# Optimization experiments

Hardware: AMD Instinct MI355X
Metric: run time of the kernel (lower is better)

## Reference

```python
import jax, jax.numpy as jnp
import numpy as np

TEMP = 0.05
BG_KNN = 50
POSK = 3
BAL_W = 0.15
P = 32768   # num proxies in memory bank
D = 256     # feature dim
C = 8       # num cameras (proxy p has camera p % C, pseudo-label p // C)
N = 65536   # dataset size
B = 256     # batch


def setup_inputs() -> dict:
    key = jax.random.key(0)
    k1, k2, k3, k4 = jax.random.split(key, 4)
    mem = jax.random.normal(k1, (P, D), jnp.float32)
    mem = mem / jnp.linalg.norm(mem, axis=1, keepdims=True)  # L2-normalized bank
    features = jax.random.normal(k2, (B, D), jnp.float32)
    all_proxy_label = jax.random.randint(k3, (N,), 0, P, jnp.int32)
    all_pseudo_label = all_proxy_label // C          # consistent with label_proxies layout
    targets = jax.random.randint(k4, (B,), 0, N, jnp.int32)
    cams = all_proxy_label[targets] % C              # each sample's camera owns its target proxy
    Pc = P // C
    cam_proxies = (jnp.arange(C)[:, None] + C * jnp.arange(Pc)[None, :]).astype(jnp.int32)   # [C, Pc]
    label_proxies = (jnp.arange(P // C)[:, None] * C + jnp.arange(C)[None, :]).astype(jnp.int32)  # [num_ids, C]
    return dict(features=features, targets=targets, cams=cams, epoch=0,
                global_memory=mem, all_pseudo_label=all_pseudo_label,
                all_proxy_label=all_proxy_label, cam_proxies=cam_proxies,
                label_proxies=label_proxies)


def _cam_mean_sum(per_sample, cams, num_cams):
    # original: for each camera, mean loss over that camera's samples, then sum over cameras
    s = jax.ops.segment_sum(per_sample, cams, num_segments=num_cams)
    n = jax.ops.segment_sum(jnp.ones_like(per_sample), cams, num_segments=num_cams)
    return jnp.where(n > 0, s / jnp.maximum(n, 1.0), 0.0).sum()


def _forward(features, global_memory, targets, cams, all_pseudo_label,
             all_proxy_label, cam_proxies, label_proxies):
    pseudo_y = all_pseudo_label[targets]      # [B]
    prx = all_proxy_label[targets]            # [B]
    num_cams = cam_proxies.shape[0]
    Bsz = features.shape[0]
    rows = jnp.arange(Bsz)

    # ExemplarMemory: score = features @ memory^T; backward treats memory as constant
    score = features @ jax.lax.stop_gradient(global_memory).T   # [B, P]
    inputs = score / TEMP

    # --- intra-camera loss: log-softmax over this sample's camera proxies ---
    cam_prx = cam_proxies[cams]                                   # [B, Pc]
    sel = jnp.take_along_axis(inputs, cam_prx, axis=1)            # [B, Pc]
    mask = (cam_prx == prx[:, None]).astype(inputs.dtype)
    intra = -(jax.nn.log_softmax(sel, axis=1) * mask).sum(axis=1)

    # --- cross-camera proxy-associate loss: positives + bg_knn hardest negatives ---
    pos = label_proxies[pseudo_y]                                 # [B, K]
    K = pos.shape[1]
    temp = jax.lax.stop_gradient(inputs).at[rows[:, None], pos].set(10000.0)
    _, top_idx = jax.lax.top_k(temp, BG_KNN + K)                  # descending: positives first
    sel2 = jnp.take_along_axis(inputs, top_idx, axis=1)           # [B, bg_knn+K]
    tgt2 = jnp.concatenate([jnp.full((K,), 1.0 / K, inputs.dtype),
                            jnp.zeros((BG_KNN,), inputs.dtype)])
    cross = -(jax.nn.log_softmax(sel2, axis=1) * tgt2).sum(axis=1)

    # --- online camera-wise NN-enhance loss ---
    mem = jax.lax.stop_gradient(global_memory)
    sims = BAL_W * jax.lax.stop_gradient(score) + (1.0 - BAL_W) * (mem[prx] @ mem.T)  # [B, P]
    sims_by_cam = sims[:, cam_proxies]                            # [B, C, Pc]
    arg = jnp.argmax(sims_by_cam, axis=2)                         # [B, C] best proxy per camera
    tops = cam_proxies[jnp.arange(num_cams)[None, :], arg]        # [B, C]
    top_vals = jnp.take_along_axis(sims, tops, axis=1)            # [B, C]
    _, sel_c = jax.lax.top_k(top_vals, POSK)                      # posK strongest camera-tops
    chosen = jnp.take_along_axis(tops, sel_c, axis=1)             # [B, posK]
    sims = sims.at[rows[:, None], chosen].set(10000.0)
    _, top3 = jax.lax.top_k(sims, BG_KNN + POSK)                  # positives first (descending)
    sel3 = jnp.take_along_axis(inputs, top3, axis=1)
    tgt3 = jnp.concatenate([jnp.full((POSK,), 1.0 / POSK, inputs.dtype),
                            jnp.zeros((BG_KNN,), inputs.dtype)])
    online = -(jax.nn.log_softmax(sel3, axis=1) * tgt3).sum(axis=1)

    return (_cam_mean_sum(intra, cams, num_cams)
            + _cam_mean_sum(cross, cams, num_cams)
            + _cam_mean_sum(online, cams, num_cams))


def reference(features, targets, cams, epoch, global_memory, all_pseudo_label,
              all_proxy_label, cam_proxies, label_proxies):
    return _forward(features, global_memory, targets, cams,
                    all_pseudo_label, all_proxy_label, cam_proxies, label_proxies)
```

## Files before the change

kernel.cpp:

```cpp
#include <hip/hip_runtime.h>

#define P_CNT 32768
#define D_DIM 256
#define B_SZ  256
#define NTHR  1024
#define NW    16
#define INVT  20.0f
#define NEG_BIG -3.0e38f

typedef _Float16 half8  __attribute__((ext_vector_type(8)));
typedef _Float16 half4v __attribute__((ext_vector_type(4)));
typedef float    floatx4 __attribute__((ext_vector_type(4)));

__device__ __forceinline__ float blockMax(float v, int tid, float* redW) {
#pragma unroll
  for (int off = 1; off < 64; off <<= 1) v = fmaxf(v, __shfl_xor(v, off));
  if ((tid & 63) == 0) redW[tid >> 6] = v;
  __syncthreads();
  float r = redW[0];
#pragma unroll
  for (int w = 1; w < NW; ++w) r = fmaxf(r, redW[w]);
  __syncthreads();
  return r;
}

__device__ __forceinline__ float blockSum(float v, int tid, float* redW) {
#pragma unroll
  for (int off = 1; off < 64; off <<= 1) v += __shfl_xor(v, off);
  if ((tid & 63) == 0) redW[tid >> 6] = v;
  __syncthreads();
  float r = 0.f;
#pragma unroll
  for (int w = 0; w < NW; ++w) r += redW[w];
  __syncthreads();
  return r;
}

template <typename GetV>
__device__ __forceinline__ float histSelectK(GetV getv, int k, int tid,
                                             int* hist , int* wt ,
                                             int* ibc , float* bufV ,
                                             int* cntS, float* bcast) {
  const int lane = tid & 63, wid = tid >> 6;
  int shift = 19, prevShift = 32;
  unsigned prefix = 0;
  int krem = k;
  for (;;) {
    {
      int4* h4 = (int4*)hist;
      h4[tid] = make_int4(0, 0, 0, 0);
      h4[tid + 1024] = make_int4(0, 0, 0, 0);
    }
    __syncthreads();
#pragma unroll
    for (int j = 0; j < 32; ++j) {
      float v = getv(j);
      unsigned bu = __float_as_uint(v);
      unsigned key = bu ^ ((unsigned)(((int)bu) >> 31) | 0x80000000u);
      bool ok = (prevShift >= 32) || ((key >> prevShift) == prefix);
      if (ok) atomicAdd(&hist[(key >> shift) & 8191], 1);
    }
    __syncthreads();
    int bcnt[8];
    int L = 0;
#pragma unroll
    for (int j = 0; j < 8; ++j) { bcnt[j] = hist[8 * tid + j]; L += bcnt[j]; }
    int S = L;
#pragma unroll
    for (int off = 1; off < 64; off <<= 1) {
      int y = __shfl_down(S, off);
      S += (lane + off < 64) ? y : 0;
    }
    if (lane == 0) wt[wid] = S;
    __syncthreads();
    int aboveW = 0;
    for (int w = wid + 1; w < NW; ++w) aboveW += wt[w];
    const int R = S + aboveW;
    const int aboveR = R - L;
    if (aboveR < krem && krem <= R) {
      int above = aboveR;
      int bsel = -1, csel = 0;
#pragma unroll
      for (int j = 7; j >= 0; --j) {
        if (bsel < 0) {
          if (above + bcnt[j] >= krem) { bsel = 8 * tid + j; csel = bcnt[j]; }
          else above += bcnt[j];
        }
      }
      ibc[0] = bsel; ibc[1] = krem - above; ibc[2] = csel;
    }
    __syncthreads();
    const int bstar = ibc[0];
    krem = ibc[1];
    const int cntT = ibc[2];
    __syncthreads();
    const int gap = prevShift - shift;
    prefix = (prefix << gap) | ((unsigned)bstar & ((1u << gap) - 1u));
    prevShift = shift;
    if (cntT <= 64 || shift == 0) break;
    shift = (shift >= 13) ? (shift - 13) : 0;
  }
  if (tid == 0) cntS[0] = 0;
  __syncthreads();
#pragma unroll
  for (int j = 0; j < 32; ++j) {
    float v = getv(j);
    unsigned bu = __float_as_uint(v);
    unsigned key = bu ^ ((unsigned)(((int)bu) >> 31) | 0x80000000u);
    if ((key >> prevShift) == prefix) {
      int p = atomicAdd(cntS, 1);
      if (p < 64) bufV[p] = v;
    }
  }
  __syncthreads();
  if (tid < 64) {
    int n = min(cntS[0], 64);
    float vl = (tid < n) ? bufV[tid] : NEG_BIG;
    float vkv = NEG_BIG;
    for (int it = 0; it < krem; ++it) {
      float wv = vl;
#pragma unroll
      for (int off = 1; off < 64; off <<= 1) wv = fmaxf(wv, __shfl_xor(wv, off));
      if (it == krem - 1) vkv = wv;
      unsigned long long m = __ballot(vl == wv);
      int fl = (int)__ffsll(m) - 1;
      if (tid == fl) vl = NEG_BIG;
    }
    if (tid == 0) bcast[0] = vkv;
  }
  __syncthreads();
  float r = bcast[0];
  __syncthreads();
  return r;
}

__global__ void prep_kernel(const float* __restrict__ features,
                            const int* __restrict__ targets,
                            const int* __restrict__ all_prx,
                            const float* __restrict__ mem,
                            float* __restrict__ A2,
                            int* __restrict__ prxArr) {
  const int b = blockIdx.x;
  const int k = threadIdx.x;
  const int t = targets[b];
  const int pr = all_prx[t];
  if (k == 0) prxArr[b] = pr;
  A2[b * D_DIM + k] = features[b * D_DIM + k];
  A2[(B_SZ + b) * D_DIM + k] = mem[(size_t)pr * D_DIM + k];
}

__global__ __launch_bounds__(256) void gemm_mfma(const float* __restrict__ A,
                                                 const float* __restrict__ Bm,
                                                 float* __restrict__ Co) {
  __shared__ _Float16 Ah[128][32], Al[128][32], Bh[128][32], Bl[128][32];
  const int tid = threadIdx.x;
  const int lane = tid & 63;
  const int wid = tid >> 6;
  const int wr = wid >> 1, wc = wid & 1;
  const int orig = (blockIdx.x & 7) * 128 + (blockIdx.x >> 3);
  const int rowBase = (orig & 3) << 7;
  const int colBase = (orig >> 2) << 7;

  const int trow = tid >> 3;
  const int tseg = tid & 7;

  floatx4 acc[4][4];
#pragma unroll
  for (int i = 0; i < 4; ++i)
#pragma unroll
    for (int j = 0; j < 4; ++j) {
      acc[i][j][0] = 0.f; acc[i][j][1] = 0.f; acc[i][j][2] = 0.f; acc[i][j][3] = 0.f;
    }

  const int fr = lane & 15;
  const int kg = (lane >> 4) << 3;

  for (int step = 0; step < 8; ++step) {
    const int k0 = step << 5;
    float4 sa[4], sb[4];
#pragma unroll
    for (int p = 0; p < 4; ++p) {
      const int r = trow + (p << 5);
      sa[p] = *(const float4*)(A  + (size_t)(rowBase + r) * D_DIM + k0 + tseg * 4);
      sb[p] = *(const float4*)(Bm + (size_t)(colBase + r) * D_DIM + k0 + tseg * 4);
    }
    __syncthreads();
#pragma unroll
    for (int p = 0; p < 4; ++p) {
      const int r = trow + (p << 5);
      float4 v = sa[p];
      half4v h, l;
      h[0] = (_Float16)v.x; l[0] = (_Float16)(v.x - (float)h[0]);
      h[1] = (_Float16)v.y; l[1] = (_Float16)(v.y - (float)h[1]);
      h[2] = (_Float16)v.z; l[2] = (_Float16)(v.z - (float)h[2]);
      h[3] = (_Float16)v.w; l[3] = (_Float16)(v.w - (float)h[3]);
      *(half4v*)&Ah[r][tseg * 4] = h;
      *(half4v*)&Al[r][tseg * 4] = l;
      v = sb[p];
      h[0] = (_Float16)v.x; l[0] = (_Float16)(v.x - (float)h[0]);
      h[1] = (_Float16)v.y; l[1] = (_Float16)(v.y - (float)h[1]);
      h[2] = (_Float16)v.z; l[2] = (_Float16)(v.z - (float)h[2]);
      h[3] = (_Float16)v.w; l[3] = (_Float16)(v.w - (float)h[3]);
      *(half4v*)&Bh[r][tseg * 4] = h;
      *(half4v*)&Bl[r][tseg * 4] = l;
    }
    __syncthreads();
    half8 ah[4], al[4], bh[4], bl[4];
#pragma unroll
    for (int f = 0; f < 4; ++f) {
      ah[f] = *(const half8*)&Ah[wr * 64 + f * 16 + fr][kg];
      al[f] = *(const half8*)&Al[wr * 64 + f * 16 + fr][kg];
      bh[f] = *(const half8*)&Bh[wc * 64 + f * 16 + fr][kg];
      bl[f] = *(const half8*)&Bl[wc * 64 + f * 16 + fr][kg];
    }
#pragma unroll
    for (int fm = 0; fm < 4; ++fm)
#pragma unroll
      for (int fn = 0; fn < 4; ++fn) {
        acc[fm][fn] = __builtin_amdgcn_mfma_f32_16x16x32_f16(ah[fm], bh[fn], acc[fm][fn], 0, 0, 0);
        acc[fm][fn] = __builtin_amdgcn_mfma_f32_16x16x32_f16(ah[fm], bl[fn], acc[fm][fn], 0, 0, 0);
        acc[fm][fn] = __builtin_amdgcn_mfma_f32_16x16x32_f16(al[fm], bh[fn], acc[fm][fn], 0, 0, 0);
      }
  }
  const int rsub = (lane >> 4) << 2;
#pragma unroll
  for (int fm = 0; fm < 4; ++fm)
#pragma unroll
    for (int fn = 0; fn < 4; ++fn) {
      const int r0 = rowBase + wr * 64 + fm * 16 + rsub;
      const int c0 = colBase + wc * 64 + fn * 16 + fr;
#pragma unroll
      for (int r = 0; r < 4; ++r)
        Co[(size_t)(r0 + r) * P_CNT + c0] = acc[fm][fn][r];
    }
}

__global__ __launch_bounds__(NTHR) void persample(const float* __restrict__ OUT,
                                                  const int* __restrict__ cams,
                                                  const int* __restrict__ prxArr,
                                                  float* __restrict__ intraArr,
                                                  float* __restrict__ crossArr,
                                                  float* __restrict__ onlArr) {
  __shared__ int   hist[8192];
  __shared__ int   wt[NW];
  __shared__ int   ibc[4];
  __shared__ float bufV[64];
  __shared__ int   bufI[32];
  __shared__ int   cntS[4];
  __shared__ float redW[NW];
  __shared__ float sv[64];
  __shared__ int   si[64];
  __shared__ float cvW[NW * 8];
  __shared__ int   ciW[NW * 8];
  __shared__ float mw[NW], sw[NW];
  __shared__ float bcast[2];

  const int b = blockIdx.x;
  const int tid = threadIdx.x;
  const int lane = tid & 63, wid = tid >> 6;
  const float* Srow = OUT + (size_t)b * P_CNT;
  const float* Mrow = OUT + (size_t)(B_SZ + b) * P_CNT;
  const int pr = prxArr[b];
  const int cam = cams[b];
  const int base4 = tid << 2;

  float s[32];
#pragma unroll
  for (int q = 0; q < 8; ++q) {
    float4 f = ((const float4*)Srow)[tid + (q << 10)];
    s[4 * q + 0] = f.x; s[4 * q + 1] = f.y; s[4 * q + 2] = f.z; s[4 * q + 3] = f.w;
  }
  float pmax = NEG_BIG;
#pragma unroll
  for (int j = 0; j < 32; ++j) pmax = fmaxf(pmax, s[j]);
  const float M = blockMax(pmax, tid, redW);

  {
    const bool mine = ((tid & 1) == (cam >> 2));
    const int cc = cam & 3;
    float im = NEG_BIG, is = 0.f;
    if (mine) {
#pragma unroll
      for (int q = 0; q < 8; ++q) {
        float v = (cc == 0) ? s[4 * q] : (cc == 1) ? s[4 * q + 1]
                : (cc == 2) ? s[4 * q + 2] : s[4 * q + 3];
        if (v <= im) is += expf((v - im) * INVT);
        else { is = is * expf((im - v) * INVT) + 1.f; im = v; }
      }
    }
#pragma unroll
    for (int off = 1; off < 64; off <<= 1) {
      float m2 = __shfl_xor(im, off);
      float s2 = __shfl_xor(is, off);
      float Mx = fmaxf(im, m2);
      is = is * expf((im - Mx) * INVT) + s2 * expf((m2 - Mx) * INVT);
      im = Mx;
    }
    if (lane == 0) { mw[wid] = im; sw[wid] = is; }
  }
  __syncthreads();
  if (tid == 0) {
    float m0 = mw[0], s0 = sw[0];
    for (int w = 1; w < NW; ++w) {
      float Mx = fmaxf(m0, mw[w]);
      s0 = s0 * expf((m0 - Mx) * INVT) + sw[w] * expf((mw[w] - Mx) * INVT);
      m0 = Mx;
    }
    intraArr[b] = -((Srow[pr] - m0) * INVT - logf(s0));
  }

  const int posBase = pr & ~7;
  if (tid < 8) sv[tid] = Srow[posBase + tid];
  __syncthreads();
  auto crossVal = [&](int j) -> float {
    int p = base4 + ((j >> 2) << 12) + (j & 3);
    return ((unsigned)(p - posBase) < 8u) ? NEG_BIG : s[j];
  };
  const float vk = histSelectK(crossVal, 50, tid, hist, wt, ibc, bufV, cntS, bcast);
  {
    float se = 0.f, cg = 0.f;
#pragma unroll
    for (int j = 0; j < 32; ++j) {
      float v = crossVal(j);
      if (v > vk) { se += expf((v - M) * INVT); cg += 1.f; }
    }
    se = blockSum(se, tid, redW);
    cg = blockSum(cg, tid, redW);
    if (tid == 0) {
      float stot = se + (50.f - cg) * expf((vk - M) * INVT);
      for (int p = 0; p < 8; ++p) stot += expf((sv[p] - M) * INVT);
      float lse = logf(stot);
      float acc = 0.f;
      for (int p = 0; p < 8; ++p) acc += (sv[p] - M) * INVT - lse;
      crossArr[b] = -acc * 0.125f;
    }
  }

#pragma unroll
  for (int q = 0; q < 8; ++q) {
    float4 m2 = ((const float4*)Mrow)[tid + (q << 10)];
    s[4 * q + 0] = 0.15f * s[4 * q + 0] + 0.85f * m2.x;
    s[4 * q + 1] = 0.15f * s[4 * q + 1] + 0.85f * m2.y;
    s[4 * q + 2] = 0.15f * s[4 * q + 2] + 0.85f * m2.z;
    s[4 * q + 3] = 0.15f * s[4 * q + 3] + 0.85f * m2.w;
  }

  {
    float cm[4] = {NEG_BIG, NEG_BIG, NEG_BIG, NEG_BIG};
    int cix[4] = {0x7fffffff, 0x7fffffff, 0x7fffffff, 0x7fffffff};
#pragma unroll
    for (int q = 0; q < 8; ++q) {
#pragma unroll
      for (int c = 0; c < 4; ++c) {
        float v = s[4 * q + c];
        int p = base4 + (q << 12) + c;
        if (v > cm[c]) { cm[c] = v; cix[c] = p; }
      }
    }
    const bool odd = (tid & 1);
    float v8[8]; int i8[8];
#pragma unroll
    for (int c = 0; c < 4; ++c) {
      float ov = __shfl_xor(cm[c], 1); int oi = __shfl_xor(cix[c], 1);
      v8[c]     = odd ? ov : cm[c];   i8[c]     = odd ? oi : cix[c];
      v8[c + 4] = odd ? cm[c] : ov;   i8[c + 4] = odd ? cix[c] : oi;
    }
#pragma unroll
    for (int off = 2; off <= 32; off <<= 1) {
#pragma unroll
      for (int c = 0; c < 8; ++c) {
        float vv = __shfl_xor(v8[c], off);
        int   ii = __shfl_xor(i8[c], off);
        if (vv > v8[c] || (vv == v8[c] && ii < i8[c])) { v8[c] = vv; i8[c] = ii; }
      }
    }
    if (lane < 8) {
#pragma unroll
      for (int c = 0; c < 8; ++c)
        if (lane == c) { cvW[wid * 8 + c] = v8[c]; ciW[wid * 8 + c] = i8[c]; }
    }
    __syncthreads();
    if (tid < 8) {
      float v = cvW[tid]; int ix = ciW[tid];
      for (int w = 1; w < NW; ++w) {
        float v2 = cvW[w * 8 + tid]; int i2 = ciW[w * 8 + tid];
        if (v2 > v || (v2 == v && i2 < ix)) { v = v2; ix = i2; }
      }
      cvW[tid] = v; ciW[tid] = ix;
    }
    __syncthreads();
    if (tid == 0) {
      unsigned used = 0;
      for (int k = 0; k < 3; ++k) {
        float best = NEG_BIG; int bc = 0;
        for (int c = 0; c < 8; ++c)
          if (!((used >> c) & 1u) && cvW[c] > best) { best = cvW[c]; bc = c; }
        used |= 1u << bc;
        si[k] = ciW[bc];
      }
    }
    __syncthreads();
  }
  const int c0 = si[0], c1 = si[1], c2 = si[2];
  __syncthreads();

  auto simsVal = [&](int j) -> float {
    int p = base4 + ((j >> 2) << 12) + (j & 3);
    return (p == c0 || p == c1 || p == c2) ? NEG_BIG : s[j];
  };
  const float vk2 = histSelectK(simsVal, 50, tid, hist, wt, ibc, bufV, cntS, bcast);
  if (tid == 0) { cntS[1] = 0; cntS[2] = 0; }
  __syncthreads();
#pragma unroll
  for (int j = 0; j < 32; ++j) {
    float v = simsVal(j);
    int p = base4 + ((j >> 2) << 12) + (j & 3);
    if (v > vk2) {
      int t = atomicAdd(&cntS[1], 1);
      if (t < 50) si[3 + t] = p;
    } else if (v == vk2) {
      int t = atomicAdd(&cntS[2], 1);
      if (t < 32) bufI[t] = p;
    }
  }
  __syncthreads();
  {
    const int cg = cntS[1];
    const int fill = 50 - cg;
    if (tid < 64) {
      int ne = min(cntS[2], 32);
      int il = (tid < ne) ? bufI[tid] : 0x7fffffff;
      for (int it = 0; it < fill; ++it) {
        int wi = il;
#pragma unroll
        for (int off = 1; off < 64; off <<= 1) wi = min(wi, __shfl_xor(wi, off));
        if (tid == 0) si[3 + cg + it] = wi;
        if (il == wi) il = 0x7fffffff;
      }
    }
  }
  __syncthreads();
  if (tid < 53) sv[tid] = Srow[si[tid]];
  __syncthreads();
  if (tid < 64) {
    float v = (tid < 53) ? sv[tid] : NEG_BIG;
    float mm = v;
#pragma unroll
    for (int off = 1; off < 64; off <<= 1) mm = fmaxf(mm, __shfl_xor(mm, off));
    float e = (tid < 53) ? expf((v - mm) * INVT) : 0.f;
    float ss = e;
#pragma unroll
    for (int off = 1; off < 64; off <<= 1) ss += __shfl_xor(ss, off);
    float lse = logf(ss);
    float c = (tid < 3) ? ((v - mm) * INVT - lse) : 0.f;
#pragma unroll
    for (int off = 1; off < 64; off <<= 1) c += __shfl_xor(c, off);
    if (tid == 0) onlArr[b] = -c * (1.0f / 3.0f);
  }
}

__global__ void finalize(const int* __restrict__ cams,
                         const float* __restrict__ ia,
                         const float* __restrict__ ca,
                         const float* __restrict__ oa,
                         float* __restrict__ out) {
  if (blockIdx.x == 0 && threadIdx.x == 0) {
    float s[8] = {}; float n[8] = {};
    for (int b = 0; b < B_SZ; ++b) {
      int c = cams[b];
      s[c] += ia[b] + ca[b] + oa[b];
      n[c] += 1.f;
    }
    float tot = 0.f;
    for (int c = 0; c < 8; ++c)
      if (n[c] > 0.f) tot += s[c] / n[c];
    out[0] = tot;
  }
}

extern "C" void kernel_launch(void* const* d_in, const int* in_sizes, int n_in,
                              void* d_out, int out_size, void* d_ws, size_t ws_size,
                              hipStream_t stream) {
  const float* features = (const float*)d_in[0];
  const int*   targets  = (const int*)d_in[1];
  const int*   cams     = (const int*)d_in[2];
  const float* mem      = (const float*)d_in[4];
  const int*   all_prx  = (const int*)d_in[6];

  float* ws = (float*)d_ws;
  float* A2  = ws;
  float* OUT = ws + 512 * D_DIM;
  float* tail = OUT + (size_t)512 * P_CNT;
  int*   prxArr  = (int*)tail;
  float* intraArr = (float*)(prxArr + B_SZ);
  float* crossArr = intraArr + B_SZ;
  float* onlArr   = crossArr + B_SZ;

  prep_kernel<<<B_SZ, D_DIM, 0, stream>>>(features, targets, all_prx, mem, A2, prxArr);
  gemm_mfma<<<1024, 256, 0, stream>>>(A2, mem, OUT);
  persample<<<B_SZ, NTHR, 0, stream>>>(OUT, cams, prxArr, intraArr, crossArr, onlArr);
  finalize<<<1, 64, 0, stream>>>(cams, intraArr, crossArr, onlArr, (float*)d_out);
}
```

Baseline: 143.7 us.

## Fuse top-k threshold selection with candidate gathering to cut block syncs

Splits the histogram radix select so it returns only the target bin prefix. The final pass then gathers above-bin elements directly and the in-bin candidates into shared buffers. The k-th value is resolved by a one-wave rank count over at most 64 candidates instead of a serial extract-max loop. This drops one full 32-element rescan per selection and several block-wide barriers and reductions, and the online loss tail now runs within a single wave. A reader note: the in-wave write to si followed by reading Srow[si[tid]] relies on wave-level ordering of shared memory without a barrier, and candidates beyond 64 are silently dropped.

```diff
diff --git a/kernel.cpp b/kernel.cpp
--- a/kernel.cpp
+++ b/kernel.cpp
@@ -36,27 +36,29 @@
   return r;
 }
 
+__device__ __forceinline__ unsigned fkey(float v) {
+  unsigned bu = __float_as_uint(v);
+  return bu ^ ((unsigned)(((int)bu) >> 31) | 0x80000000u);
+}
+
 template <typename GetV>
-__device__ __forceinline__ float histSelectK(GetV getv, int k, int tid,
-                                             int* hist , int* wt ,
-                                             int* ibc , float* bufV ,
-                                             int* cntS, float* bcast) {
+__device__ __forceinline__ void histFindBin(GetV getv, int k, int tid,
+                                            int* hist , int* wt ,
+                                            int* ibc ,
+                                            unsigned& prefixOut, int& prevShiftOut,
+                                            int& kremOut) {
   const int lane = tid & 63, wid = tid >> 6;
   int shift = 19, prevShift = 32;
   unsigned prefix = 0;
   int krem = k;
   for (;;) {
-    {
-      int4* h4 = (int4*)hist;
-      h4[tid] = make_int4(0, 0, 0, 0);
-      h4[tid + 1024] = make_int4(0, 0, 0, 0);
-    }
+    int4* h4 = (int4*)hist;
+    h4[tid] = make_int4(0, 0, 0, 0);
+    h4[tid + 1024] = make_int4(0, 0, 0, 0);
     __syncthreads();
 #pragma unroll
     for (int j = 0; j < 32; ++j) {
-      float v = getv(j);
-      unsigned bu = __float_as_uint(v);
-      unsigned key = bu ^ ((unsigned)(((int)bu) >> 31) | 0x80000000u);
+      unsigned key = fkey(getv(j));
       bool ok = (prevShift >= 32) || ((key >> prevShift) == prefix);
       if (ok) atomicAdd(&hist[(key >> shift) & 8191], 1);
     }
@@ -93,45 +95,14 @@
     const int bstar = ibc[0];
     krem = ibc[1];
     const int cntT = ibc[2];
-    __syncthreads();
     const int gap = prevShift - shift;
     prefix = (prefix << gap) | ((unsigned)bstar & ((1u << gap) - 1u));
     prevShift = shift;
     if (cntT <= 64 || shift == 0) break;
     shift = (shift >= 13) ? (shift - 13) : 0;
-  }
-  if (tid == 0) cntS[0] = 0;
-  __syncthreads();
-#pragma unroll
-  for (int j = 0; j < 32; ++j) {
-    float v = getv(j);
-    unsigned bu = __float_as_uint(v);
-    unsigned key = bu ^ ((unsigned)(((int)bu) >> 31) | 0x80000000u);
-    if ((key >> prevShift) == prefix) {
-      int p = atomicAdd(cntS, 1);
-      if (p < 64) bufV[p] = v;
-    }
-  }
-  __syncthreads();
-  if (tid < 64) {
-    int n = min(cntS[0], 64);
-    float vl = (tid < n) ? bufV[tid] : NEG_BIG;
-    float vkv = NEG_BIG;
-    for (int it = 0; it < krem; ++it) {
-      float wv = vl;
-#pragma unroll
-      for (int off = 1; off < 64; off <<= 1) wv = fmaxf(wv, __shfl_xor(wv, off));
-      if (it == krem - 1) vkv = wv;
-      unsigned long long m = __ballot(vl == wv);
-      int fl = (int)__ffsll(m) - 1;
-      if (tid == fl) vl = NEG_BIG;
-    }
-    if (tid == 0) bcast[0] = vkv;
-  }
-  __syncthreads();
-  float r = bcast[0];
-  __syncthreads();
-  return r;
+    __syncthreads();
+  }
+  prefixOut = prefix; prevShiftOut = prevShift; kremOut = krem;
 }
 
 __global__ void prep_kernel(const float* __restrict__ features,
@@ -245,7 +216,7 @@
   __shared__ int   wt[NW];
   __shared__ int   ibc[4];
   __shared__ float bufV[64];
-  __shared__ int   bufI[32];
+  __shared__ int   bufI[64];
   __shared__ int   cntS[4];
   __shared__ float redW[NW];
   __shared__ float sv[64];
@@ -253,7 +224,6 @@
   __shared__ float cvW[NW * 8];
   __shared__ int   ciW[NW * 8];
   __shared__ float mw[NW], sw[NW];
-  __shared__ float bcast[2];
 
   const int b = blockIdx.x;
   const int tid = threadIdx.x;
@@ -298,6 +268,8 @@
     }
     if (lane == 0) { mw[wid] = im; sw[wid] = is; }
   }
+  const int posBase = pr & ~7;
+  if (tid < 8) sv[tid] = Srow[posBase + tid];
   __syncthreads();
   if (tid == 0) {
     float m0 = mw[0], s0 = sw[0];
@@ -309,30 +281,51 @@
     intraArr[b] = -((Srow[pr] - m0) * INVT - logf(s0));
   }
 
-  const int posBase = pr & ~7;
-  if (tid < 8) sv[tid] = Srow[posBase + tid];
-  __syncthreads();
   auto crossVal = [&](int j) -> float {
     int p = base4 + ((j >> 2) << 12) + (j & 3);
     return ((unsigned)(p - posBase) < 8u) ? NEG_BIG : s[j];
   };
-  const float vk = histSelectK(crossVal, 50, tid, hist, wt, ibc, bufV, cntS, bcast);
   {
-    float se = 0.f, cg = 0.f;
+    unsigned prefix; int prevShift, krem;
+    histFindBin(crossVal, 50, tid, hist, wt, ibc, prefix, prevShift, krem);
+    if (tid == 0) cntS[0] = 0;
+    __syncthreads();
+    float seAbove = 0.f;
 #pragma unroll
     for (int j = 0; j < 32; ++j) {
       float v = crossVal(j);
-      if (v > vk) { se += expf((v - M) * INVT); cg += 1.f; }
-    }
-    se = blockSum(se, tid, redW);
-    cg = blockSum(cg, tid, redW);
-    if (tid == 0) {
-      float stot = se + (50.f - cg) * expf((vk - M) * INVT);
-      for (int p = 0; p < 8; ++p) stot += expf((sv[p] - M) * INVT);
-      float lse = logf(stot);
-      float acc = 0.f;
-      for (int p = 0; p < 8; ++p) acc += (sv[p] - M) * INVT - lse;
-      crossArr[b] = -acc * 0.125f;
+      unsigned keyTop = fkey(v) >> prevShift;
+      if (keyTop > prefix) seAbove += expf((v - M) * INVT);
+      else if (keyTop == prefix) {
+        int p = atomicAdd(&cntS[0], 1);
+        if (p < 64) bufV[p] = v;
+      }
+    }
+    seAbove = blockSum(seAbove, tid, redW);
+    if (tid < 64) {
+      const int n = min(cntS[0], 64);
+      const bool valid = (tid < n);
+      float vl = valid ? bufV[tid] : NEG_BIG;
+      int r = 0, eq = 0;
+      for (int m2 = 0; m2 < 64; ++m2) {
+        float vm = (m2 < n) ? bufV[m2] : NEG_BIG;
+        r += (vm > vl); eq += (vm == vl);
+      }
+      unsigned long long mb = __ballot(valid && r < krem && krem <= r + eq);
+      int selLane = (mb == 0) ? 0 : (int)__ffsll(mb) - 1;
+      float vk = __shfl(vl, selLane);
+      int rAbove = __shfl(r, selLane);
+      float e = (valid && vl > vk) ? expf((vl - M) * INVT) : 0.f;
+#pragma unroll
+      for (int off = 1; off < 64; off <<= 1) e += __shfl_xor(e, off);
+      if (tid == 0) {
+        float stot = seAbove + e + (float)(krem - rAbove) * expf((vk - M) * INVT);
+        float acc = 0.f;
+        for (int p = 0; p < 8; ++p) stot += expf((sv[p] - M) * INVT);
+        float lse = logf(stot);
+        for (int p = 0; p < 8; ++p) acc += (sv[p] - M) * INVT - lse;
+        crossArr[b] = -acc * 0.125f;
+      }
     }
   }
 
@@ -408,54 +401,62 @@
     int p = base4 + ((j >> 2) << 12) + (j & 3);
     return (p == c0 || p == c1 || p == c2) ? NEG_BIG : s[j];
   };
-  const float vk2 = histSelectK(simsVal, 50, tid, hist, wt, ibc, bufV, cntS, bcast);
-  if (tid == 0) { cntS[1] = 0; cntS[2] = 0; }
-  __syncthreads();
-#pragma unroll
-  for (int j = 0; j < 32; ++j) {
-    float v = simsVal(j);
-    int p = base4 + ((j >> 2) << 12) + (j & 3);
-    if (v > vk2) {
-      int t = atomicAdd(&cntS[1], 1);
-      if (t < 50) si[3 + t] = p;
-    } else if (v == vk2) {
-      int t = atomicAdd(&cntS[2], 1);
-      if (t < 32) bufI[t] = p;
-    }
-  }
-  __syncthreads();
   {
-    const int cg = cntS[1];
-    const int fill = 50 - cg;
+    unsigned prefix; int prevShift, krem;
+    histFindBin(simsVal, 50, tid, hist, wt, ibc, prefix, prevShift, krem);
+    if (tid == 0) { cntS[0] = 0; cntS[1] = 3; }
+    __syncthreads();
+#pragma unroll
+    for (int j = 0; j < 32; ++j) {
+      float v = simsVal(j);
+      int p = base4 + ((j >> 2) << 12) + (j & 3);
+      unsigned keyTop = fkey(v) >> prevShift;
+      if (keyTop > prefix) {
+        int t = atomicAdd(&cntS[1], 1);
+        si[t] = p;
+      } else if (keyTop == prefix) {
+        int t = atomicAdd(&cntS[0], 1);
+        if (t < 64) { bufV[t] = v; bufI[t] = p; }
+      }
+    }
+    __syncthreads();
     if (tid < 64) {
-      int ne = min(cntS[2], 32);
-      int il = (tid < ne) ? bufI[tid] : 0x7fffffff;
-      for (int it = 0; it < fill; ++it) {
-        int wi = il;
-#pragma unroll
-        for (int off = 1; off < 64; off <<= 1) wi = min(wi, __shfl_xor(wi, off));
-        if (tid == 0) si[3 + cg + it] = wi;
-        if (il == wi) il = 0x7fffffff;
-      }
-    }
-  }
-  __syncthreads();
-  if (tid < 53) sv[tid] = Srow[si[tid]];
-  __syncthreads();
-  if (tid < 64) {
-    float v = (tid < 53) ? sv[tid] : NEG_BIG;
-    float mm = v;
-#pragma unroll
-    for (int off = 1; off < 64; off <<= 1) mm = fmaxf(mm, __shfl_xor(mm, off));
-    float e = (tid < 53) ? expf((v - mm) * INVT) : 0.f;
-    float ss = e;
-#pragma unroll
-    for (int off = 1; off < 64; off <<= 1) ss += __shfl_xor(ss, off);
-    float lse = logf(ss);
-    float c = (tid < 3) ? ((v - mm) * INVT - lse) : 0.f;
-#pragma unroll
-    for (int off = 1; off < 64; off <<= 1) c += __shfl_xor(c, off);
-    if (tid == 0) onlArr[b] = -c * (1.0f / 3.0f);
+      const int n = min(cntS[0], 64);
+      const bool valid = (tid < n);
+      float vl = valid ? bufV[tid] : NEG_BIG;
+      int il = valid ? bufI[tid] : 0x7fffffff;
+      int r = 0, eq = 0, ti = 0;
+      for (int m2 = 0; m2 < 64; ++m2) {
+        float vm = (m2 < n) ? bufV[m2] : NEG_BIG;
+        int im = (m2 < n) ? bufI[m2] : 0x7fffffff;
+        r += (vm > vl); eq += (vm == vl);
+        ti += (vm == vl && im < il);
+      }
+      unsigned long long mb = __ballot(valid && r < krem && krem <= r + eq);
+      int selLane = (mb == 0) ? 0 : (int)__ffsll(mb) - 1;
+      float vk = __shfl(vl, selLane);
+      int rAbove = __shfl(r, selLane);
+      int tcnt = krem - rAbove;
+      bool take = valid && ((vl > vk) || (vl == vk && ti < tcnt));
+      if (take) {
+        int t = atomicAdd(&cntS[1], 1);
+        si[t] = il;
+      }
+      float v = NEG_BIG;
+      if (tid < 53) v = Srow[si[tid]];
+      float mm = v;
+#pragma unroll
+      for (int off = 1; off < 64; off <<= 1) mm = fmaxf(mm, __shfl_xor(mm, off));
+      float e = (tid < 53) ? expf((v - mm) * INVT) : 0.f;
+      float ss = e;
+#pragma unroll
+      for (int off = 1; off < 64; off <<= 1) ss += __shfl_xor(ss, off);
+      float lse = logf(ss);
+      float c = (tid < 3) ? ((v - mm) * INVT - lse) : 0.f;
+#pragma unroll
+      for (int off = 1; off < 64; off <<= 1) c += __shfl_xor(c, off);
+      if (tid == 0) onlArr[b] = -c * (1.0f / 3.0f);
+    }
   }
 }
 
```

New measurement: 162.6 us. 1.13x slower.

## Split per-sample selection into sliced candidate collection plus merge kernel

Applied to the files above, without the earlier changes.

The single 1024-thread per-sample kernel becomes two stages. The first runs 8 slice blocks per sample and computes partial max and intra-camera logsumexp plus per-camera argmax. It also collects top-K candidates with an adaptive 256-bin value histogram that starts from a guessed range below the slice max. The second kernel merges the slice candidates with a rank-count sort to finish the cross and online losses. This spreads work over more, smaller blocks and replaces the multi-pass radix select, but it relies on value-range heuristics and a fixed candidate cap (128), which could drop correct top-K entries on other data.

```diff
diff --git a/kernel.cpp b/kernel.cpp
--- a/kernel.cpp
+++ b/kernel.cpp
@@ -3,135 +3,105 @@
 #define P_CNT 32768
 #define D_DIM 256
 #define B_SZ  256
-#define NTHR  1024
-#define NW    16
 #define INVT  20.0f
 #define NEG_BIG -3.0e38f
+#define SLICE_N 4096
+#define NSLICE 8
+#define CAP 128
 
 typedef _Float16 half8  __attribute__((ext_vector_type(8)));
 typedef _Float16 half4v __attribute__((ext_vector_type(4)));
 typedef float    floatx4 __attribute__((ext_vector_type(4)));
 
-__device__ __forceinline__ float blockMax(float v, int tid, float* redW) {
+__device__ __forceinline__ float blockMax4(float v, int tid, float* red4) {
 #pragma unroll
   for (int off = 1; off < 64; off <<= 1) v = fmaxf(v, __shfl_xor(v, off));
-  if ((tid & 63) == 0) redW[tid >> 6] = v;
-  __syncthreads();
-  float r = redW[0];
-#pragma unroll
-  for (int w = 1; w < NW; ++w) r = fmaxf(r, redW[w]);
+  if ((tid & 63) == 0) red4[tid >> 6] = v;
+  __syncthreads();
+  float r = fmaxf(fmaxf(red4[0], red4[1]), fmaxf(red4[2], red4[3]));
   __syncthreads();
   return r;
 }
 
-__device__ __forceinline__ float blockSum(float v, int tid, float* redW) {
+__device__ __forceinline__ float blockSum4(float v, int tid, float* red4) {
 #pragma unroll
   for (int off = 1; off < 64; off <<= 1) v += __shfl_xor(v, off);
-  if ((tid & 63) == 0) redW[tid >> 6] = v;
-  __syncthreads();
-  float r = 0.f;
-#pragma unroll
-  for (int w = 0; w < NW; ++w) r += redW[w];
+  if ((tid & 63) == 0) red4[tid >> 6] = v;
+  __syncthreads();
+  float r = red4[0] + red4[1] + red4[2] + red4[3];
   __syncthreads();
   return r;
 }
 
-template <typename GetV>
-__device__ __forceinline__ float histSelectK(GetV getv, int k, int tid,
-                                             int* hist , int* wt ,
-                                             int* ibc , float* bufV ,
-                                             int* cntS, float* bcast) {
-  const int lane = tid & 63, wid = tid >> 6;
-  int shift = 19, prevShift = 32;
-  unsigned prefix = 0;
-  int krem = k;
-  for (;;) {
-    {
-      int4* h4 = (int4*)hist;
-      h4[tid] = make_int4(0, 0, 0, 0);
-      h4[tid + 1024] = make_int4(0, 0, 0, 0);
-    }
-    __syncthreads();
-#pragma unroll
-    for (int j = 0; j < 32; ++j) {
+template <typename GetV, typename GetI>
+__device__ void selectCollect(GetV getv, GetI geti, int K, float hi, float range0,
+                              int tid, int lane,
+                              int* hist, int* ibc, int* lcnt,
+                              float* oVal, int* oIdx, int* oCnt) {
+  float range = range0;
+  for (int guard = 0; guard < 10; ++guard) {
+    const float lo = hi - range;
+    const float scale = 256.0f / range;
+    hist[tid] = 0;
+    if (tid == 0) ibc[0] = -1;
+    __syncthreads();
+#pragma unroll
+    for (int j = 0; j < 16; ++j) {
       float v = getv(j);
-      unsigned bu = __float_as_uint(v);
-      unsigned key = bu ^ ((unsigned)(((int)bu) >> 31) | 0x80000000u);
-      bool ok = (prevShift >= 32) || ((key >> prevShift) == prefix);
-      if (ok) atomicAdd(&hist[(key >> shift) & 8191], 1);
-    }
-    __syncthreads();
-    int bcnt[8];
-    int L = 0;
-#pragma unroll
-    for (int j = 0; j < 8; ++j) { bcnt[j] = hist[8 * tid + j]; L += bcnt[j]; }
-    int S = L;
-#pragma unroll
-    for (int off = 1; off < 64; off <<= 1) {
-      int y = __shfl_down(S, off);
-      S += (lane + off < 64) ? y : 0;
-    }
-    if (lane == 0) wt[wid] = S;
-    __syncthreads();
-    int aboveW = 0;
-    for (int w = wid + 1; w < NW; ++w) aboveW += wt[w];
-    const int R = S + aboveW;
-    const int aboveR = R - L;
-    if (aboveR < krem && krem <= R) {
-      int above = aboveR;
-      int bsel = -1, csel = 0;
-#pragma unroll
-      for (int j = 7; j >= 0; --j) {
-        if (bsel < 0) {
-          if (above + bcnt[j] >= krem) { bsel = 8 * tid + j; csel = bcnt[j]; }
-          else above += bcnt[j];
+      float t = (v - lo) * scale;
+      int bin = (int)fminf(fmaxf(t, 0.0f), 255.0f);
+      if (bin >= 1) atomicAdd(&hist[bin], 1);
+    }
+    __syncthreads();
+    if (tid < 64) {
+      int4 h = ((const int4*)hist)[tid];
+      if (tid == 0) h.x = 0;
+      int L = h.x + h.y + h.z + h.w;
+      int S = L;
+#pragma unroll
+      for (int off = 1; off < 64; off <<= 1) {
+        int y = __shfl_down(S, off);
+        S += (lane + off < 64) ? y : 0;
+      }
+      int total = __shfl(S, 0);
+      if (total >= K) {
+        int above = S - L;
+        if (above < K && S >= K) {
+          int a = above, bsel;
+          if (a + h.w >= K) bsel = 4 * tid + 3;
+          else { a += h.w;
+            if (a + h.z >= K) bsel = 4 * tid + 2;
+            else { a += h.z;
+              if (a + h.y >= K) bsel = 4 * tid + 1;
+              else bsel = 4 * tid;
+            } }
+          ibc[0] = bsel;
         }
       }
-      ibc[0] = bsel; ibc[1] = krem - above; ibc[2] = csel;
-    }
-    __syncthreads();
-    const int bstar = ibc[0];
-    krem = ibc[1];
-    const int cntT = ibc[2];
-    __syncthreads();
-    const int gap = prevShift - shift;
-    prefix = (prefix << gap) | ((unsigned)bstar & ((1u << gap) - 1u));
-    prevShift = shift;
-    if (cntT <= 64 || shift == 0) break;
-    shift = (shift >= 13) ? (shift - 13) : 0;
-  }
-  if (tid == 0) cntS[0] = 0;
-  __syncthreads();
-#pragma unroll
-  for (int j = 0; j < 32; ++j) {
-    float v = getv(j);
-    unsigned bu = __float_as_uint(v);
-    unsigned key = bu ^ ((unsigned)(((int)bu) >> 31) | 0x80000000u);
-    if ((key >> prevShift) == prefix) {
-      int p = atomicAdd(cntS, 1);
-      if (p < 64) bufV[p] = v;
-    }
-  }
-  __syncthreads();
-  if (tid < 64) {
-    int n = min(cntS[0], 64);
-    float vl = (tid < n) ? bufV[tid] : NEG_BIG;
-    float vkv = NEG_BIG;
-    for (int it = 0; it < krem; ++it) {
-      float wv = vl;
-#pragma unroll
-      for (int off = 1; off < 64; off <<= 1) wv = fmaxf(wv, __shfl_xor(wv, off));
-      if (it == krem - 1) vkv = wv;
-      unsigned long long m = __ballot(vl == wv);
-      int fl = (int)__ffsll(m) - 1;
-      if (tid == fl) vl = NEG_BIG;
-    }
-    if (tid == 0) bcast[0] = vkv;
-  }
-  __syncthreads();
-  float r = bcast[0];
-  __syncthreads();
-  return r;
+    }
+    __syncthreads();
+    if (ibc[0] >= 0) {
+      const int Bstar = ibc[0];
+      if (tid == 0) *lcnt = 0;
+      __syncthreads();
+#pragma unroll
+      for (int j = 0; j < 16; ++j) {
+        float v = getv(j);
+        float t = (v - lo) * scale;
+        int bin = (int)fminf(fmaxf(t, 0.0f), 255.0f);
+        if (bin >= Bstar) {
+          int tt = atomicAdd(lcnt, 1);
+          if (tt < CAP) { oVal[tt] = v; oIdx[tt] = geti(j); }
+        }
+      }
+      __syncthreads();
+      if (tid == 0) *oCnt = min(*lcnt, CAP);
+      return;
+    }
+    range *= 4.0f;
+    __syncthreads();
+  }
+  if (tid == 0) *oCnt = 0;
 }
 
 __global__ void prep_kernel(const float* __restrict__ features,
@@ -235,45 +205,40 @@
     }
 }
 
-__global__ __launch_bounds__(NTHR) void persample(const float* __restrict__ OUT,
-                                                  const int* __restrict__ cams,
-                                                  const int* __restrict__ prxArr,
-                                                  float* __restrict__ intraArr,
-                                                  float* __restrict__ crossArr,
-                                                  float* __restrict__ onlArr) {
-  __shared__ int   hist[8192];
-  __shared__ int   wt[NW];
-  __shared__ int   ibc[4];
-  __shared__ float bufV[64];
-  __shared__ int   bufI[32];
-  __shared__ int   cntS[4];
-  __shared__ float redW[NW];
-  __shared__ float sv[64];
-  __shared__ int   si[64];
-  __shared__ float cvW[NW * 8];
-  __shared__ int   ciW[NW * 8];
-  __shared__ float mw[NW], sw[NW];
-  __shared__ float bcast[2];
-
-  const int b = blockIdx.x;
-  const int tid = threadIdx.x;
-  const int lane = tid & 63, wid = tid >> 6;
-  const float* Srow = OUT + (size_t)b * P_CNT;
-  const float* Mrow = OUT + (size_t)(B_SZ + b) * P_CNT;
-  const int pr = prxArr[b];
-  const int cam = cams[b];
-  const int base4 = tid << 2;
-
-  float s[32];
-#pragma unroll
-  for (int q = 0; q < 8; ++q) {
-    float4 f = ((const float4*)Srow)[tid + (q << 10)];
-    s[4 * q + 0] = f.x; s[4 * q + 1] = f.y; s[4 * q + 2] = f.z; s[4 * q + 3] = f.w;
-  }
-  float pmax = NEG_BIG;
-#pragma unroll
-  for (int j = 0; j < 32; ++j) pmax = fmaxf(pmax, s[j]);
-  const float M = blockMax(pmax, tid, redW);
+__global__ __launch_bounds__(256) void persample1(
+    const float* __restrict__ OUT, const int* __restrict__ cams,
+    const int* __restrict__ prxArr,
+    float* __restrict__ pmaxA, float* __restrict__ imA, float* __restrict__ isA,
+    float* __restrict__ camV, int* __restrict__ camI,
+    int* __restrict__ cxCnt, float* __restrict__ cxVal, int* __restrict__ cxIdx,
+    int* __restrict__ smCnt, float* __restrict__ smVal, int* __restrict__ smIdx) {
+  __shared__ __align__(16) int hist[256];
+  __shared__ int ibc[2];
+  __shared__ int lcnt;
+  __shared__ float red4[4];
+  __shared__ float mwS[4], swS[4];
+  __shared__ float cvW[32]; __shared__ int ciW[32];
+
+  const int blk = blockIdx.x;
+  const int b = blk >> 3, s = blk & 7;
+  const int tid = threadIdx.x, lane = tid & 63, wid = tid >> 6;
+  const int sl = b * NSLICE + s;
+  const float* Srow = OUT + (size_t)b * P_CNT + s * SLICE_N;
+  const float* Mrow = OUT + (size_t)(B_SZ + b) * P_CNT + s * SLICE_N;
+  const int pr = prxArr[b], cam = cams[b];
+  const int gbase = s * SLICE_N + 4 * tid;
+
+  float sc[16];
+#pragma unroll
+  for (int q = 0; q < 4; ++q) {
+    float4 f = ((const float4*)Srow)[tid + 256 * q];
+    sc[4 * q + 0] = f.x; sc[4 * q + 1] = f.y; sc[4 * q + 2] = f.z; sc[4 * q + 3] = f.w;
+  }
+  float mx = sc[0];
+#pragma unroll
+  for (int j = 1; j < 16; ++j) mx = fmaxf(mx, sc[j]);
+  const float Mslice = blockMax4(mx, tid, red4);
+  if (tid == 0) pmaxA[sl] = Mslice;
 
   {
     const bool mine = ((tid & 1) == (cam >> 2));
@@ -281,9 +246,9 @@
     float im = NEG_BIG, is = 0.f;
     if (mine) {
 #pragma unroll
-      for (int q = 0; q < 8; ++q) {
-        float v = (cc == 0) ? s[4 * q] : (cc == 1) ? s[4 * q + 1]
-                : (cc == 2) ? s[4 * q + 2] : s[4 * q + 3];
+      for (int q = 0; q < 4; ++q) {
+        float v = (cc == 0) ? sc[4 * q] : (cc == 1) ? sc[4 * q + 1]
+                : (cc == 2) ? sc[4 * q + 2] : sc[4 * q + 3];
         if (v <= im) is += expf((v - im) * INVT);
         else { is = is * expf((im - v) * INVT) + 1.f; im = v; }
       }
@@ -296,67 +261,51 @@
       is = is * expf((im - Mx) * INVT) + s2 * expf((m2 - Mx) * INVT);
       im = Mx;
     }
-    if (lane == 0) { mw[wid] = im; sw[wid] = is; }
-  }
-  __syncthreads();
-  if (tid == 0) {
-    float m0 = mw[0], s0 = sw[0];
-    for (int w = 1; w < NW; ++w) {
-      float Mx = fmaxf(m0, mw[w]);
-      s0 = s0 * expf((m0 - Mx) * INVT) + sw[w] * expf((mw[w] - Mx) * INVT);
-      m0 = Mx;
-    }
-    intraArr[b] = -((Srow[pr] - m0) * INVT - logf(s0));
+    if (lane == 0) { mwS[wid] = im; swS[wid] = is; }
+    __syncthreads();
+    if (tid == 0) {
+      float m0 = mwS[0], s0 = swS[0];
+      for (int w = 1; w < 4; ++w) {
+        float Mx = fmaxf(m0, mwS[w]);
+        s0 = s0 * expf((m0 - Mx) * INVT) + swS[w] * expf((mwS[w] - Mx) * INVT);
+        m0 = Mx;
+      }
+      imA[sl] = m0; isA[sl] = s0;
+    }
+    __syncthreads();
   }
 
   const int posBase = pr & ~7;
-  if (tid < 8) sv[tid] = Srow[posBase + tid];
-  __syncthreads();
-  auto crossVal = [&](int j) -> float {
-    int p = base4 + ((j >> 2) << 12) + (j & 3);
-    return ((unsigned)(p - posBase) < 8u) ? NEG_BIG : s[j];
+  auto cval = [&](int j) -> float {
+    int p = gbase + ((j >> 2) << 10) + (j & 3);
+    return ((unsigned)(p - posBase) < 8u) ? NEG_BIG : sc[j];
   };
-  const float vk = histSelectK(crossVal, 50, tid, hist, wt, ibc, bufV, cntS, bcast);
+  auto gidx = [&](int j) -> int { return gbase + ((j >> 2) << 10) + (j & 3); };
+  selectCollect(cval, gidx, 53, Mslice, 2.0f, tid, lane, hist, ibc, &lcnt,
+                cxVal + (size_t)sl * CAP, cxIdx + (size_t)sl * CAP, cxCnt + sl);
+
+  float sm[16];
+#pragma unroll
+  for (int q = 0; q < 4; ++q) {
+    float4 g = ((const float4*)Mrow)[tid + 256 * q];
+    sm[4 * q + 0] = 0.15f * sc[4 * q + 0] + 0.85f * g.x;
+    sm[4 * q + 1] = 0.15f * sc[4 * q + 1] + 0.85f * g.y;
+    sm[4 * q + 2] = 0.15f * sc[4 * q + 2] + 0.85f * g.z;
+    sm[4 * q + 3] = 0.15f * sc[4 * q + 3] + 0.85f * g.w;
+  }
+
   {
-    float se = 0.f, cg = 0.f;
-#pragma unroll
-    for (int j = 0; j < 32; ++j) {
-      float v = crossVal(j);
-      if (v > vk) { se += expf((v - M) * INVT); cg += 1.f; }
-    }
-    se = blockSum(se, tid, redW);
-    cg = blockSum(cg, tid, redW);
-    if (tid == 0) {
-      float stot = se + (50.f - cg) * expf((vk - M) * INVT);
-      for (int p = 0; p < 8; ++p) stot += expf((sv[p] - M) * INVT);
-      float lse = logf(stot);
-      float acc = 0.f;
-      for (int p = 0; p < 8; ++p) acc += (sv[p] - M) * INVT - lse;
-      crossArr[b] = -acc * 0.125f;
-    }
-  }
-
-#pragma unroll
-  for (int q = 0; q < 8; ++q) {
-    float4 m2 = ((const float4*)Mrow)[tid + (q << 10)];
-    s[4 * q + 0] = 0.15f * s[4 * q + 0] + 0.85f * m2.x;
-    s[4 * q + 1] = 0.15f * s[4 * q + 1] + 0.85f * m2.y;
-    s[4 * q + 2] = 0.15f * s[4 * q + 2] + 0.85f * m2.z;
-    s[4 * q + 3] = 0.15f * s[4 * q + 3] + 0.85f * m2.w;
-  }
-
-  {
-    float cm[4] = {NEG_BIG, NEG_BIG, NEG_BIG, NEG_BIG};
-    int cix[4] = {0x7fffffff, 0x7fffffff, 0x7fffffff, 0x7fffffff};
-#pragma unroll
-    for (int q = 0; q < 8; ++q) {
+    float cm[4]; int cix[4];
+#pragma unroll
+    for (int c = 0; c < 4; ++c) { cm[c] = NEG_BIG; cix[c] = 0x7fffffff; }
+#pragma unroll
+    for (int q = 0; q < 4; ++q)
 #pragma unroll
       for (int c = 0; c < 4; ++c) {
-        float v = s[4 * q + c];
-        int p = base4 + (q << 12) + c;
+        float v = sm[4 * q + c];
+        int p = gbase + (q << 10) + c;
         if (v > cm[c]) { cm[c] = v; cix[c] = p; }
       }
-    }
     const bool odd = (tid & 1);
     float v8[8]; int i8[8];
 #pragma unroll
@@ -366,14 +315,12 @@
       v8[c + 4] = odd ? cm[c] : ov;   i8[c + 4] = odd ? cix[c] : oi;
     }
 #pragma unroll
-    for (int off = 2; off <= 32; off <<= 1) {
+    for (int off = 2; off <= 32; off <<= 1)
 #pragma unroll
       for (int c = 0; c < 8; ++c) {
-        float vv = __shfl_xor(v8[c], off);
-        int   ii = __shfl_xor(i8[c], off);
+        float vv = __shfl_xor(v8[c], off); int ii = __shfl_xor(i8[c], off);
         if (vv > v8[c] || (vv == v8[c] && ii < i8[c])) { v8[c] = vv; i8[c] = ii; }
       }
-    }
     if (lane < 8) {
 #pragma unroll
       for (int c = 0; c < 8; ++c)
@@ -382,80 +329,200 @@
     __syncthreads();
     if (tid < 8) {
       float v = cvW[tid]; int ix = ciW[tid];
-      for (int w = 1; w < NW; ++w) {
+      for (int w = 1; w < 4; ++w) {
         float v2 = cvW[w * 8 + tid]; int i2 = ciW[w * 8 + tid];
         if (v2 > v || (v2 == v && i2 < ix)) { v = v2; ix = i2; }
       }
-      cvW[tid] = v; ciW[tid] = ix;
-    }
-    __syncthreads();
+      camV[(size_t)sl * 8 + tid] = v; camI[(size_t)sl * 8 + tid] = ix;
+    }
+    __syncthreads();
+  }
+
+  float mx2 = sm[0];
+#pragma unroll
+  for (int j = 1; j < 16; ++j) mx2 = fmaxf(mx2, sm[j]);
+  const float Ms = blockMax4(mx2, tid, red4);
+  auto sval = [&](int j) -> float { return sm[j]; };
+  selectCollect(sval, gidx, 56, Ms, 0.35f, tid, lane, hist, ibc, &lcnt,
+                smVal + (size_t)sl * CAP, smIdx + (size_t)sl * CAP, smCnt + sl);
+}
+
+__global__ __launch_bounds__(256) void persample2(
+    const float* __restrict__ OUT, const int* __restrict__ prxArr,
+    const float* __restrict__ pmaxA, const float* __restrict__ imA,
+    const float* __restrict__ isA,
+    const float* __restrict__ camV, const int* __restrict__ camI,
+    const int* __restrict__ cxCnt, const float* __restrict__ cxVal,
+    const int* __restrict__ cxIdx,
+    const int* __restrict__ smCnt, const float* __restrict__ smVal,
+    const int* __restrict__ smIdx,
+    float* __restrict__ intraArr, float* __restrict__ crossArr,
+    float* __restrict__ onlArr) {
+  __shared__ float vbuf[NSLICE * CAP];
+  __shared__ int   ibuf[NSLICE * CAP];
+  __shared__ int   offs[9];
+  __shared__ float red4[4];
+  __shared__ float MM[1];
+  __shared__ float cv[8]; __shared__ int ci[8];
+  __shared__ int   ch[3];
+  __shared__ float sbuf[56];
+  __shared__ int   scnt;
+
+  const int b = blockIdx.x;
+  const int tid = threadIdx.x;
+  const float* Srow = OUT + (size_t)b * P_CNT;
+  const int pr = prxArr[b];
+  const int posBase = pr & ~7;
+
+  if (tid < 8) {
+    float v = pmaxA[b * NSLICE + tid];
+#pragma unroll
+    for (int off = 1; off < 8; off <<= 1) v = fmaxf(v, __shfl_xor(v, off));
+    if (tid == 0) MM[0] = v;
+  }
+  if (tid == 32) {
+    int o = 0;
+    for (int s = 0; s < NSLICE; ++s) { offs[s] = o; o += cxCnt[b * NSLICE + s]; }
+    offs[8] = o;
+  }
+  if (tid == 64) {
+    float m0 = imA[b * NSLICE], s0 = isA[b * NSLICE];
+    for (int s = 1; s < NSLICE; ++s) {
+      float m2 = imA[b * NSLICE + s], s2 = isA[b * NSLICE + s];
+      float Mx = fmaxf(m0, m2);
+      s0 = s0 * expf((m0 - Mx) * INVT) + s2 * expf((m2 - Mx) * INVT);
+      m0 = Mx;
+    }
+    intraArr[b] = -((Srow[pr] - m0) * INVT - logf(s0));
+  }
+  __syncthreads();
+  const float M = MM[0];
+  const int C = offs[8];
+
+  for (int s = 0; s < NSLICE; ++s) {
+    int o = offs[s], n = offs[s + 1] - o;
+    for (int i = tid; i < n; i += 256) {
+      vbuf[o + i] = cxVal[(size_t)(b * NSLICE + s) * CAP + i];
+      ibuf[o + i] = cxIdx[(size_t)(b * NSLICE + s) * CAP + i];
+    }
+  }
+  __syncthreads();
+  {
+    float ve[4]; int ie[4]; int rk[4];
+#pragma unroll
+    for (int k = 0; k < 4; ++k) {
+      int e = tid + 256 * k;
+      ve[k] = (e < C) ? vbuf[e] : NEG_BIG;
+      ie[k] = (e < C) ? ibuf[e] : 0x7fffffff;
+      rk[k] = 0;
+    }
+    for (int m = 0; m < C; ++m) {
+      float vm = vbuf[m]; int im = ibuf[m];
+#pragma unroll
+      for (int k = 0; k < 4; ++k)
+        rk[k] += (vm > ve[k]) || (vm == ve[k] && im < ie[k]);
+    }
+    float myexp = 0.f;
+#pragma unroll
+    for (int k = 0; k < 4; ++k) {
+      int e = tid + 256 * k;
+      if (e < C && rk[k] < 50) myexp += expf((ve[k] - M) * INVT);
+    }
+    float pe = 0.f, pl = 0.f;
+    if (tid < 8) {
+      float pv = Srow[posBase + tid];
+      pe = expf((pv - M) * INVT);
+      pl = (pv - M) * INVT;
+    }
+    float stot = blockSum4(myexp + pe, tid, red4);
+    float plin = blockSum4(pl, tid, red4);
     if (tid == 0) {
-      unsigned used = 0;
-      for (int k = 0; k < 3; ++k) {
-        float best = NEG_BIG; int bc = 0;
-        for (int c = 0; c < 8; ++c)
-          if (!((used >> c) & 1u) && cvW[c] > best) { best = cvW[c]; bc = c; }
-        used |= 1u << bc;
-        si[k] = ciW[bc];
-      }
-    }
-    __syncthreads();
-  }
-  const int c0 = si[0], c1 = si[1], c2 = si[2];
-  __syncthreads();
-
-  auto simsVal = [&](int j) -> float {
-    int p = base4 + ((j >> 2) << 12) + (j & 3);
-    return (p == c0 || p == c1 || p == c2) ? NEG_BIG : s[j];
-  };
-  const float vk2 = histSelectK(simsVal, 50, tid, hist, wt, ibc, bufV, cntS, bcast);
-  if (tid == 0) { cntS[1] = 0; cntS[2] = 0; }
-  __syncthreads();
-#pragma unroll
-  for (int j = 0; j < 32; ++j) {
-    float v = simsVal(j);
-    int p = base4 + ((j >> 2) << 12) + (j & 3);
-    if (v > vk2) {
-      int t = atomicAdd(&cntS[1], 1);
-      if (t < 50) si[3 + t] = p;
-    } else if (v == vk2) {
-      int t = atomicAdd(&cntS[2], 1);
-      if (t < 32) bufI[t] = p;
+      float lse = logf(stot);
+      crossArr[b] = -(plin - 8.f * lse) * 0.125f;
+    }
+  }
+
+  if (tid < 8) {
+    float v = camV[(size_t)(b * NSLICE) * 8 + tid];
+    int  ix = camI[(size_t)(b * NSLICE) * 8 + tid];
+    for (int s = 1; s < NSLICE; ++s) {
+      float v2 = camV[(size_t)(b * NSLICE + s) * 8 + tid];
+      int  i2 = camI[(size_t)(b * NSLICE + s) * 8 + tid];
+      if (v2 > v || (v2 == v && i2 < ix)) { v = v2; ix = i2; }
+    }
+    cv[tid] = v; ci[tid] = ix;
+  }
+  if (tid == 32) {
+    int o = 0;
+    for (int s = 0; s < NSLICE; ++s) { offs[s] = o; o += smCnt[b * NSLICE + s]; }
+    offs[8] = o;
+  }
+  __syncthreads();
+  if (tid == 0) {
+    unsigned used = 0;
+    for (int k = 0; k < 3; ++k) {
+      float best = NEG_BIG; int bc = 0;
+      for (int c = 0; c < 8; ++c)
+        if (!((used >> c) & 1u) && cv[c] > best) { best = cv[c]; bc = c; }
+      used |= 1u << bc;
+      ch[k] = ci[bc];
+    }
+    scnt = 0;
+  }
+  __syncthreads();
+  const int c0 = ch[0], c1 = ch[1], c2 = ch[2];
+  const int C2 = offs[8];
+
+  for (int s = 0; s < NSLICE; ++s) {
+    int o = offs[s], n = offs[s + 1] - o;
+    for (int i = tid; i < n; i += 256) {
+      float v = smVal[(size_t)(b * NSLICE + s) * CAP + i];
+      int  ix = smIdx[(size_t)(b * NSLICE + s) * CAP + i];
+      if (ix == c0 || ix == c1 || ix == c2) v = NEG_BIG;
+      vbuf[o + i] = v; ibuf[o + i] = ix;
     }
   }
   __syncthreads();
   {
-    const int cg = cntS[1];
-    const int fill = 50 - cg;
+    float ve[4]; int ie[4]; int rk[4];
+#pragma unroll
+    for (int k = 0; k < 4; ++k) {
+      int e = tid + 256 * k;
+      ve[k] = (e < C2) ? vbuf[e] : NEG_BIG;
+      ie[k] = (e < C2) ? ibuf[e] : 0x7fffffff;
+      rk[k] = 0;
+    }
+    for (int m = 0; m < C2; ++m) {
+      float vm = vbuf[m]; int im = ibuf[m];
+#pragma unroll
+      for (int k = 0; k < 4; ++k)
+        rk[k] += (vm > ve[k]) || (vm == ve[k] && im < ie[k]);
+    }
+#pragma unroll
+    for (int k = 0; k < 4; ++k) {
+      int e = tid + 256 * k;
+      if (e < C2 && ve[k] > -1.0e38f && rk[k] < 50) {
+        int t = atomicAdd(&scnt, 1);
+        if (t < 50) sbuf[t] = Srow[ie[k]];
+      }
+    }
+    if (tid < 3) sbuf[50 + tid] = Srow[ch[tid]];
+    __syncthreads();
     if (tid < 64) {
-      int ne = min(cntS[2], 32);
-      int il = (tid < ne) ? bufI[tid] : 0x7fffffff;
-      for (int it = 0; it < fill; ++it) {
-        int wi = il;
-#pragma unroll
-        for (int off = 1; off < 64; off <<= 1) wi = min(wi, __shfl_xor(wi, off));
-        if (tid == 0) si[3 + cg + it] = wi;
-        if (il == wi) il = 0x7fffffff;
-      }
-    }
-  }
-  __syncthreads();
-  if (tid < 53) sv[tid] = Srow[si[tid]];
-  __syncthreads();
-  if (tid < 64) {
-    float v = (tid < 53) ? sv[tid] : NEG_BIG;
-    float mm = v;
-#pragma unroll
-    for (int off = 1; off < 64; off <<= 1) mm = fmaxf(mm, __shfl_xor(mm, off));
-    float e = (tid < 53) ? expf((v - mm) * INVT) : 0.f;
-    float ss = e;
-#pragma unroll
-    for (int off = 1; off < 64; off <<= 1) ss += __shfl_xor(ss, off);
-    float lse = logf(ss);
-    float c = (tid < 3) ? ((v - mm) * INVT - lse) : 0.f;
-#pragma unroll
-    for (int off = 1; off < 64; off <<= 1) c += __shfl_xor(c, off);
-    if (tid == 0) onlArr[b] = -c * (1.0f / 3.0f);
+      float v = (tid < 53) ? sbuf[tid] : NEG_BIG;
+      float mm = v;
+#pragma unroll
+      for (int off = 1; off < 64; off <<= 1) mm = fmaxf(mm, __shfl_xor(mm, off));
+      float e = (tid < 53) ? expf((v - mm) * INVT) : 0.f;
+      float ss = e;
+#pragma unroll
+      for (int off = 1; off < 64; off <<= 1) ss += __shfl_xor(ss, off);
+      float lse = logf(ss);
+      float c = (tid >= 50 && tid < 53) ? ((v - mm) * INVT - lse) : 0.f;
+#pragma unroll
+      for (int off = 1; off < 64; off <<= 1) c += __shfl_xor(c, off);
+      if (tid == 0) onlArr[b] = -c * (1.0f / 3.0f);
+    }
   }
 }
 
@@ -490,14 +557,30 @@
   float* ws = (float*)d_ws;
   float* A2  = ws;
   float* OUT = ws + 512 * D_DIM;
-  float* tail = OUT + (size_t)512 * P_CNT;
-  int*   prxArr  = (int*)tail;
-  float* intraArr = (float*)(prxArr + B_SZ);
-  float* crossArr = intraArr + B_SZ;
-  float* onlArr   = crossArr + B_SZ;
+  char*  tail = (char*)(OUT + (size_t)512 * P_CNT);
+
+  int*   prxArr  = (int*)tail;                  tail += B_SZ * 4;
+  float* intraArr = (float*)tail;               tail += B_SZ * 4;
+  float* crossArr = (float*)tail;               tail += B_SZ * 4;
+  float* onlArr   = (float*)tail;               tail += B_SZ * 4;
+  float* pmaxA = (float*)tail;                  tail += B_SZ * NSLICE * 4;
+  float* imA   = (float*)tail;                  tail += B_SZ * NSLICE * 4;
+  float* isA   = (float*)tail;                  tail += B_SZ * NSLICE * 4;
+  float* camV  = (float*)tail;                  tail += B_SZ * NSLICE * 8 * 4;
+  int*   camI  = (int*)tail;                    tail += B_SZ * NSLICE * 8 * 4;
+  int*   cxCnt = (int*)tail;                    tail += B_SZ * NSLICE * 4;
+  int*   smCnt = (int*)tail;                    tail += B_SZ * NSLICE * 4;
+  float* cxVal = (float*)tail;                  tail += (size_t)B_SZ * NSLICE * CAP * 4;
+  int*   cxIdx = (int*)tail;                    tail += (size_t)B_SZ * NSLICE * CAP * 4;
+  float* smVal = (float*)tail;                  tail += (size_t)B_SZ * NSLICE * CAP * 4;
+  int*   smIdx = (int*)tail;                    tail += (size_t)B_SZ * NSLICE * CAP * 4;
 
   prep_kernel<<<B_SZ, D_DIM, 0, stream>>>(features, targets, all_prx, mem, A2, prxArr);
   gemm_mfma<<<1024, 256, 0, stream>>>(A2, mem, OUT);
-  persample<<<B_SZ, NTHR, 0, stream>>>(OUT, cams, prxArr, intraArr, crossArr, onlArr);
+  persample1<<<B_SZ * NSLICE, 256, 0, stream>>>(OUT, cams, prxArr,
+      pmaxA, imA, isA, camV, camI, cxCnt, cxVal, cxIdx, smCnt, smVal, smIdx);
+  persample2<<<B_SZ, 256, 0, stream>>>(OUT, prxArr,
+      pmaxA, imA, isA, camV, camI, cxCnt, cxVal, cxIdx, smCnt, smVal, smIdx,
+      intraArr, crossArr, onlArr);
   finalize<<<1, 64, 0, stream>>>(cams, intraArr, crossArr, onlArr, (float*)d_out);
 }
```

New measurement: 277.8 us. 93.3% more time.
